# Optimization experiments

Measured on AMD Instinct MI355X. Metric: run time of the kernel, lower is better.

Reference implementation:

```python
import jax, jax.numpy as jnp
import numpy as np

B, S, D = 2, 2048, 1024
H = 16
HD = D // H  # 64
SCALE = HD ** 0.5


def setup_inputs() -> dict:
    key = jax.random.key(0)
    ks = jax.random.split(key, 9)
    std = 1.0 / np.sqrt(D)
    inp = {"x": jax.random.normal(ks[0], (B, S, D), dtype=jnp.float32)}
    names = ["Wq", "Wk", "Wv", "Wo"]
    for i, n in enumerate(names):
        inp[n] = jax.random.uniform(ks[1 + i], (D, D), dtype=jnp.float32, minval=-std, maxval=std)
        inp["b" + n[1]] = jax.random.uniform(ks[5 + i], (D,), dtype=jnp.float32, minval=-std, maxval=std)
    return inp


def reference(x, Wq, Wk, Wv, Wo, bq, bk, bv, bo):
    # QKV projections (torch Linear: y = x @ W.T + b; here W stored as [in, out] already transposed)
    q = x @ Wq + bq
    k = x @ Wk + bk
    v = x @ Wv + bv
    # [B, H, S, HD]
    q = q.reshape(B, S, H, HD).transpose(0, 2, 1, 3)
    k = k.reshape(B, S, H, HD).transpose(0, 2, 1, 3)
    v = v.reshape(B, S, H, HD).transpose(0, 2, 1, 3)
    scores = jnp.einsum("bhqd,bhkd->bhqk", q, k) / SCALE  # [B, H, S, S]
    causal = jnp.tril(jnp.ones((S, S), dtype=bool))
    scores = jnp.where(causal, scores, -jnp.inf)
    attn = jax.nn.softmax(scores, axis=-1)  # dropout p=0.0 (eval)
    ctx = jnp.einsum("bhqk,bhkd->bhqd", attn, v)
    ctx = ctx.transpose(0, 2, 1, 3).reshape(B, S, D)
    return ctx @ Wo + bo
```

## Files before the change

### kernel.cpp

```cpp
#include <hip/hip_runtime.h>


#define S_LEN 2048
#define DMODEL 1024
#define NHEAD 16
#define HDIM 64
#define MROWS 4096

typedef __bf16 bf16x8 __attribute__((ext_vector_type(8)));
typedef float f32x4 __attribute__((ext_vector_type(4)));
typedef float f32x16 __attribute__((ext_vector_type(16)));

__device__ __forceinline__ ushort f2bf(float f) {
  union { float f; unsigned u; } v; v.f = f;
  unsigned r = v.u + 0x7fffu + ((v.u >> 16) & 1u);
  return (ushort)(r >> 16);
}

__device__ __forceinline__ void gload_lds16(const ushort* g, ushort* l) {
  __builtin_amdgcn_global_load_lds(
      (const __attribute__((address_space(1))) void*)g,
      (__attribute__((address_space(3))) void*)l, 16, 0, 0);
}

__device__ __forceinline__ unsigned pack2bf(float lo, float hi) {
  union { __bf16 h[2]; unsigned u; } t;
  t.h[0] = (__bf16)lo; t.h[1] = (__bf16)hi;
  return t.u;
}

#if __has_builtin(__builtin_amdgcn_permlane32_swap)
#define HAVE_PL32 1
__device__ __forceinline__ void pl32sw(unsigned& a, unsigned& b) {
  auto r = __builtin_amdgcn_permlane32_swap((int)a, (int)b, false, false);
  a = (unsigned)r[0];
  b = (unsigned)r[1];
}
#endif

__device__ __forceinline__ float halfcomb_sum(float x) {
#ifdef HAVE_PL32
  unsigned a = __float_as_uint(x), b = a;
  pl32sw(a, b);
  return __uint_as_float(a) + __uint_as_float(b);
#else
  return x + __shfl_xor(x, 32, 64);
#endif
}


__global__ __launch_bounds__(256) void cvt_x(const float* __restrict__ x,
                                             ushort* __restrict__ xb) {
  int i = (blockIdx.x * 256 + threadIdx.x) * 4;
  float4 v = *(const float4*)&x[i];
  ushort4 o;
  o.x = f2bf(v.x); o.y = f2bf(v.y); o.z = f2bf(v.z); o.w = f2bf(v.w);
  *(ushort4*)&xb[i] = o;
}

__global__ __launch_bounds__(256) void cvt_wt(const float* __restrict__ W0,
                                              const float* __restrict__ W1,
                                              const float* __restrict__ W2,
                                              const float* __restrict__ W3,
                                              ushort* __restrict__ out) {
  const float* W = blockIdx.z == 0 ? W0 : blockIdx.z == 1 ? W1
                   : blockIdx.z == 2 ? W2 : W3;
  ushort* WT = out + (size_t)blockIdx.z * DMODEL * DMODEL;
  __shared__ float tile[64][65];
  const int n0 = blockIdx.x * 64, k0 = blockIdx.y * 64;
#pragma unroll
  for (int i = 0; i < 4; ++i) {
    int chunk = i * 256 + threadIdx.x;
    int r = chunk >> 4, c4 = chunk & 15;
    float4 v = *(const float4*)&W[(size_t)(k0 + r) * DMODEL + n0 + c4 * 4];
    tile[r][c4 * 4 + 0] = v.x; tile[r][c4 * 4 + 1] = v.y;
    tile[r][c4 * 4 + 2] = v.z; tile[r][c4 * 4 + 3] = v.w;
  }
  __syncthreads();
#pragma unroll
  for (int i = 0; i < 4; ++i) {
    int chunk = i * 256 + threadIdx.x;
    int r = chunk >> 4, c4 = chunk & 15;
    ushort4 o;
    o.x = f2bf(tile[c4 * 4 + 0][r]); o.y = f2bf(tile[c4 * 4 + 1][r]);
    o.z = f2bf(tile[c4 * 4 + 2][r]); o.w = f2bf(tile[c4 * 4 + 3][r]);
    *(ushort4*)&WT[(size_t)(n0 + r) * DMODEL + k0 + c4 * 4] = o;
  }
}

__global__ __launch_bounds__(256) void trV(const ushort* __restrict__ V,
                                           ushort* __restrict__ Vt) {
  const int bh = blockIdx.z;
  const ushort* src = V + (size_t)bh * S_LEN * HDIM;
  ushort* dst = Vt + (size_t)bh * HDIM * S_LEN;
  __shared__ ushort tile[32][33];
  int s0 = blockIdx.x * 32, h0 = blockIdx.y * 32;
  int tx = threadIdx.x & 31, ty = threadIdx.x >> 5;
#pragma unroll
  for (int i = 0; i < 32; i += 8)
    tile[ty + i][tx] = src[(size_t)(s0 + ty + i) * HDIM + h0 + tx];
  __syncthreads();
#pragma unroll
  for (int i = 0; i < 32; i += 8)
    dst[(size_t)(h0 + ty + i) * S_LEN + s0 + tx] = tile[tx][ty + i];
}

__global__ __launch_bounds__(512) void gemm256(
    const ushort* __restrict__ A, const ushort* __restrict__ Bt,
    const float* __restrict__ b0, const float* __restrict__ b1,
    const float* __restrict__ b2, ushort* __restrict__ outQ,
    ushort* __restrict__ outK, ushort* __restrict__ outV) {
  const int flat = blockIdx.y * 16 + blockIdx.x;
  const int swz = (flat & 7) * 32 + (flat >> 3);
  const int bx = swz & 15, by = swz >> 4;
  const int m0 = bx * 256, n0 = by * 192;

  __shared__ __align__(16) ushort Al[2][256 * 64];
  __shared__ __align__(16) ushort Bl[2][192 * 64];

  const int tid = threadIdx.x;
  const int lane = tid & 63, wid = tid >> 6;
  const int wr = wid >> 2, wc = wid & 3;
  const int fr = lane & 15, hi16 = lane >> 4;

  f32x4 acc[8][3] = {};

#pragma unroll
  for (int l = 0; l < 4; ++l) {
    int chunk = l * 512 + tid;
    int row = chunk >> 3, cpos = chunk & 7;
    int scol = (cpos ^ (row & 7)) * 8;
    gload_lds16(&A[(size_t)(m0 + row) * DMODEL + scol], &Al[0][chunk * 8]);
  }
#pragma unroll
  for (int l = 0; l < 3; ++l) {
    int chunk = l * 512 + tid;
    int row = chunk >> 3, cpos = chunk & 7;
    int scol = (cpos ^ (row & 7)) * 8;
    gload_lds16(&Bt[(size_t)(n0 + row) * DMODEL + scol], &Bl[0][chunk * 8]);
  }
  __syncthreads();

  for (int t = 0; t < 16; ++t) {
    const int bt = t & 1;
    bf16x8 bfr[3];
#pragma unroll
    for (int s = 0; s < 4; ++s) {
      const int kk = s >> 1, mh = s & 1;
      bf16x8 af[4];
#pragma unroll
      for (int q = 0; q < 4; ++q) {
        int rl = wr * 128 + (mh * 4 + q) * 16 + fr;
        af[q] = *(const bf16x8*)&Al[bt][rl * 64 +
                                        ((kk * 4 + hi16) ^ (rl & 7)) * 8];
      }
      if (mh == 0) {
#pragma unroll
        for (int nf = 0; nf < 3; ++nf) {
          int rl = wc * 48 + nf * 16 + fr;
          bfr[nf] = *(const bf16x8*)&Bl[bt][rl * 64 +
                                            ((kk * 4 + hi16) ^ (rl & 7)) * 8];
        }
      }
      if (t + 1 < 16 && s < 2) {
        const int k64 = (t + 1) * 64;
        if (s == 0) {
#pragma unroll
          for (int l = 0; l < 4; ++l) {
            int chunk = l * 512 + tid;
            int row = chunk >> 3, cpos = chunk & 7;
            int scol = (cpos ^ (row & 7)) * 8;
            gload_lds16(&A[(size_t)(m0 + row) * DMODEL + k64 + scol],
                        &Al[bt ^ 1][chunk * 8]);
          }
        } else {
#pragma unroll
          for (int l = 0; l < 3; ++l) {
            int chunk = l * 512 + tid;
            int row = chunk >> 3, cpos = chunk & 7;
            int scol = (cpos ^ (row & 7)) * 8;
            gload_lds16(&Bt[(size_t)(n0 + row) * DMODEL + k64 + scol],
                        &Bl[bt ^ 1][chunk * 8]);
          }
        }
      }
      __builtin_amdgcn_s_barrier();
      __builtin_amdgcn_s_setprio(1);
#pragma unroll
      for (int q = 0; q < 4; ++q)
#pragma unroll
        for (int nf = 0; nf < 3; ++nf)
          acc[mh * 4 + q][nf] = __builtin_amdgcn_mfma_f32_16x16x32_bf16(
              af[q], bfr[nf], acc[mh * 4 + q][nf], 0, 0, 0);
      __builtin_amdgcn_s_setprio(0);
      if (s < 3) __builtin_amdgcn_s_barrier();
    }
    __syncthreads();
  }

#pragma unroll
  for (int mf = 0; mf < 8; ++mf) {
#pragma unroll
    for (int nf = 0; nf < 3; ++nf) {
      int col = n0 + wc * 48 + nf * 16 + fr;
      int z = col >> 10, cw = col & 1023;
      float bval = z == 0 ? b0[cw] : z == 1 ? b1[cw] : b2[cw];
      int h = cw >> 6, hd = cw & (HDIM - 1);
      ushort* dst = (z == 0) ? outQ : (z == 1) ? outK : outV;
#pragma unroll
      for (int rg = 0; rg < 4; ++rg) {
        int row = m0 + wr * 128 + mf * 16 + hi16 * 4 + rg;
        int b = row >> 11, sq = row & (S_LEN - 1);
        float val = acc[mf][nf][rg] + bval;
        dst[(((size_t)(b * NHEAD + h)) * S_LEN + sq) * HDIM + hd] = f2bf(val);
      }
    }
  }
}

__global__ __launch_bounds__(256) void gemm128o(
    const ushort* __restrict__ A, const ushort* __restrict__ Bt,
    const float* __restrict__ b0, float* __restrict__ outB) {
  const int NT = 256;
  const int flat = blockIdx.y * 32 + blockIdx.x;
  const int swz = (flat & 7) * (NT >> 3) + (flat >> 3);
  const int bx = swz & 31, by = swz >> 5;
  const int m0 = bx * 128, n0 = by * 128;

  __shared__ __align__(16) ushort Alds[2][128 * 64];
  __shared__ __align__(16) ushort Blds[2][128 * 64];

  const int tid = threadIdx.x;
  const int lane = tid & 63, w = tid >> 6;
  const int wr = w >> 1, wc = w & 1;
  const int fr = lane & 15, hi16 = lane >> 4;

  f32x4 acc[4][4] = {};

#pragma unroll
  for (int it = 0; it < 4; ++it) {
    int c = it * 256 + tid;
    int row = c >> 3;
    int sc = ((c & 7) ^ (row & 7)) * 8;
    gload_lds16(&A[(size_t)(m0 + row) * DMODEL + sc], &Alds[0][c * 8]);
    gload_lds16(&Bt[(size_t)(n0 + row) * DMODEL + sc], &Blds[0][c * 8]);
  }
  __syncthreads();

  for (int t = 0; t < 16; ++t) {
    const int bt = t & 1;
#pragma unroll
    for (int s = 0; s < 2; ++s) {
      bf16x8 af[4], bfr[4];
#pragma unroll
      for (int i = 0; i < 4; ++i) {
        int row = wr * 64 + i * 16 + fr;
        af[i] = *(const bf16x8*)&Alds[bt][row * 64 +
                                          ((s * 4 + hi16) ^ (row & 7)) * 8];
      }
#pragma unroll
      for (int j = 0; j < 4; ++j) {
        int row = wc * 64 + j * 16 + fr;
        bfr[j] = *(const bf16x8*)&Blds[bt][row * 64 +
                                           ((s * 4 + hi16) ^ (row & 7)) * 8];
      }
      if (t + 1 < 16) {
        const int k64 = (t + 1) * 64;
#pragma unroll
        for (int it = 0; it < 4; ++it) {
          int c = it * 256 + tid;
          int row = c >> 3;
          int sc = ((c & 7) ^ (row & 7)) * 8;
          if (s == 0)
            gload_lds16(&A[(size_t)(m0 + row) * DMODEL + k64 + sc],
                        &Alds[bt ^ 1][c * 8]);
          else
            gload_lds16(&Bt[(size_t)(n0 + row) * DMODEL + k64 + sc],
                        &Blds[bt ^ 1][c * 8]);
        }
      }
      __builtin_amdgcn_s_barrier();
      __builtin_amdgcn_s_setprio(1);
#pragma unroll
      for (int i = 0; i < 4; ++i)
#pragma unroll
        for (int j = 0; j < 4; ++j)
          acc[i][j] = __builtin_amdgcn_mfma_f32_16x16x32_bf16(af[i], bfr[j],
                                                              acc[i][j], 0, 0, 0);
      __builtin_amdgcn_s_setprio(0);
      if (s < 1) __builtin_amdgcn_s_barrier();
    }
    __syncthreads();
  }

#pragma unroll
  for (int i = 0; i < 4; ++i) {
#pragma unroll
    for (int j = 0; j < 4; ++j) {
      int col = n0 + wc * 64 + j * 16 + fr;
      float bval = b0[col];
#pragma unroll
      for (int r = 0; r < 4; ++r) {
        int row = m0 + wr * 64 + i * 16 + hi16 * 4 + r;
        outB[(size_t)row * DMODEL + col] = acc[i][j][r] + bval;
      }
    }
  }
}

__global__ __launch_bounds__(512, 1) void attn8(const ushort* __restrict__ Q,
                                                const ushort* __restrict__ K,
                                                const ushort* __restrict__ Vt,
                                                ushort* __restrict__ ctx) {
  const int blk = blockIdx.x;
  const int w2 = (blk & 7) * 32 + (blk >> 3);
  const int bh = w2 >> 3, ptile = w2 & 7;
  const int b = bh >> 4, h = bh & 15;
  const int tid = threadIdx.x;
  const int lane = tid & 63, wid = tid >> 6;
  const int p = wid >> 2;
  const int wq = wid & 3;
  const int q32 = lane & 31, hi = lane >> 5;
  const bool lo_half = (hi == 0);
  const int tidp = tid & 255;

  const ushort* Qb = Q + (size_t)bh * S_LEN * HDIM;
  const ushort* Kb = K + (size_t)bh * S_LEN * HDIM;
  const ushort* Vb = Vt + (size_t)bh * HDIM * S_LEN;

  __shared__ __align__(16) ushort lds[32768];
  ushort* Klp = lds;
  ushort* Vlp = lds + 16384;
  float* scr = (float*)lds;

  const float C = 0.125f * 1.44269504f;

  for (int ph = 0; ph < 2; ++ph) {
    const int T = ph ? 15 - ptile : ptile;
    const int qbase = T * 128 + wq * 32;
    const int qrow = qbase + q32;
    const int NS = T + 1;

    bf16x8 qf[4];
#pragma unroll
    for (int s = 0; s < 4; ++s)
      qf[s] = *(const bf16x8*)&Qb[(size_t)qrow * HDIM + s * 16 + hi * 8];

    f32x16 oaccA[2] = {}, oaccB[2] = {};
    float lsum = 0.f;

    {
      const int kv = p * 64;
#pragma unroll
      for (int g = 0; g < 2; ++g) {
        int chunk = g * 256 + tidp;
        int row = chunk >> 3, sc = ((chunk & 7) ^ (row & 7)) * 8;
        gload_lds16(&Kb[(size_t)(kv + row) * HDIM + sc],
                    &Klp[(p * 2 + 0) * 4096 + chunk * 8]);
        gload_lds16(&Vb[(size_t)row * S_LEN + kv + sc],
                    &Vlp[(p * 2 + 0) * 4096 + chunk * 8]);
      }
    }
    __syncthreads();

    int buf = 0;
    for (int it = 0; it < NS; ++it) {
      const int s = 2 * it + p;
      const int kv0 = s * 64;

      if (it + 1 < NS) {
        const int kvn = kv0 + 128;
#pragma unroll
        for (int g = 0; g < 2; ++g) {
          int chunk = g * 256 + tidp;
          int row = chunk >> 3, sc = ((chunk & 7) ^ (row & 7)) * 8;
          gload_lds16(&Kb[(size_t)(kvn + row) * HDIM + sc],
                      &Klp[(p * 2 + (buf ^ 1)) * 4096 + chunk * 8]);
          gload_lds16(&Vb[(size_t)row * S_LEN + kvn + sc],
                      &Vlp[(p * 2 + (buf ^ 1)) * 4096 + chunk * 8]);
        }
      }

      if (kv0 <= qbase + 31) {
        const ushort* Kt = &Klp[(p * 2 + buf) * 4096];
        const ushort* Vtl = &Vlp[(p * 2 + buf) * 4096];
        const int rsw = (q32 & 7);

        f32x16 sa[2] = {};
        __builtin_amdgcn_s_setprio(1);
#pragma unroll
        for (int sl = 0; sl < 4; ++sl) {
          bf16x8 kf0 = *(const bf16x8*)&Kt[q32 * 64 + ((sl * 2 + hi) ^ rsw) * 8];
          bf16x8 kf1 = *(const bf16x8*)&Kt[(32 + q32) * 64 +
                                           ((sl * 2 + hi) ^ rsw) * 8];
          sa[0] = __builtin_amdgcn_mfma_f32_32x32x16_bf16(kf0, qf[sl], sa[0],
                                                          0, 0, 0);
          sa[1] = __builtin_amdgcn_mfma_f32_32x32x16_bf16(kf1, qf[sl], sa[1],
                                                          0, 0, 0);
        }
        __builtin_amdgcn_s_setprio(0);

        bf16x8 vf[2][4];
#pragma unroll
        for (int t2 = 0; t2 < 2; ++t2) {
          const int row = t2 * 32 + q32;
#pragma unroll
          for (int sl = 0; sl < 4; ++sl)
            vf[t2][sl] = *(const bf16x8*)&Vtl[row * 64 +
                                              ((sl * 2 + hi) ^ rsw) * 8];
        }

        if (kv0 + 63 > qbase) {
          const int khi = kv0 + 4 * hi;
#pragma unroll
          for (int t = 0; t < 2; ++t)
#pragma unroll
            for (int rr = 0; rr < 16; ++rr) {
              int kg = khi + t * 32 + (rr & 3) + 8 * (rr >> 2);
              if (kg > qrow) sa[t][rr] = -1e30f;
            }
        }

        float psum = 0.f;
#pragma unroll
        for (int t = 0; t < 2; ++t)
#pragma unroll
          for (int rr = 0; rr < 16; ++rr) {
            float pp = __builtin_exp2f(sa[t][rr] * C);
            sa[t][rr] = pp;
            psum += pp;
          }
        lsum += halfcomb_sum(psum);

        __builtin_amdgcn_s_setprio(1);
#pragma unroll
        for (int t = 0; t < 2; ++t) {
#pragma unroll
          for (int half = 0; half < 2; ++half) {
            const int rb = half * 8;
            unsigned a0 = pack2bf(sa[t][rb + 0], sa[t][rb + 1]);
            unsigned a1 = pack2bf(sa[t][rb + 2], sa[t][rb + 3]);
            unsigned b0w = pack2bf(sa[t][rb + 4], sa[t][rb + 5]);
            unsigned b1w = pack2bf(sa[t][rb + 6], sa[t][rb + 7]);
            union { unsigned u[4]; bf16x8 v; } pf;
#ifdef HAVE_PL32
            pl32sw(a0, b0w);
            pl32sw(a1, b1w);
            pf.u[0] = a0; pf.u[1] = a1; pf.u[2] = b0w; pf.u[3] = b1w;
#else
            unsigned xa0 = __shfl_xor(a0, 32, 64);
            unsigned xa1 = __shfl_xor(a1, 32, 64);
            unsigned xb0 = __shfl_xor(b0w, 32, 64);
            unsigned xb1 = __shfl_xor(b1w, 32, 64);
            pf.u[0] = lo_half ? a0 : xb0;
            pf.u[1] = lo_half ? a1 : xb1;
            pf.u[2] = lo_half ? xa0 : b0w;
            pf.u[3] = lo_half ? xa1 : b1w;
#endif
            if (t == 0) {
              oaccA[0] = __builtin_amdgcn_mfma_f32_32x32x16_bf16(
                  vf[0][half], pf.v, oaccA[0], 0, 0, 0);
              oaccA[1] = __builtin_amdgcn_mfma_f32_32x32x16_bf16(
                  vf[1][half], pf.v, oaccA[1], 0, 0, 0);
            } else {
              oaccB[0] = __builtin_amdgcn_mfma_f32_32x32x16_bf16(
                  vf[0][2 + half], pf.v, oaccB[0], 0, 0, 0);
              oaccB[1] = __builtin_amdgcn_mfma_f32_32x32x16_bf16(
                  vf[1][2 + half], pf.v, oaccB[1], 0, 0, 0);
            }
          }
        }
        __builtin_amdgcn_s_setprio(0);
      }

      __syncthreads();
      buf ^= 1;
    }

#pragma unroll
    for (int tt = 0; tt < 2; ++tt)
#pragma unroll
      for (int rr = 0; rr < 16; ++rr) oaccA[tt][rr] += oaccB[tt][rr];

    const int base = (wq * 64 + lane) * 37;
    if (p == 1) {
      scr[base + 0] = lsum;
#pragma unroll
      for (int t = 0; t < 2; ++t)
#pragma unroll
        for (int rr = 0; rr < 16; ++rr)
          scr[base + 1 + t * 16 + rr] = oaccA[t][rr];
    }
    __syncthreads();
    if (p == 0) {
      const float lT = lsum + scr[base + 0];
      const float linv = 1.0f / lT;
      ushort* crow = &ctx[((size_t)(b * S_LEN) + qrow) * DMODEL + h * HDIM];
#pragma unroll
      for (int t = 0; t < 2; ++t)
#pragma unroll
        for (int g2 = 0; g2 < 4; ++g2) {
          ushort4 o;
          float m0 = oaccA[t][g2 * 4 + 0] + scr[base + 1 + t * 16 + g2 * 4 + 0];
          float m1 = oaccA[t][g2 * 4 + 1] + scr[base + 1 + t * 16 + g2 * 4 + 1];
          float m2 = oaccA[t][g2 * 4 + 2] + scr[base + 1 + t * 16 + g2 * 4 + 2];
          float m3 = oaccA[t][g2 * 4 + 3] + scr[base + 1 + t * 16 + g2 * 4 + 3];
          o.x = f2bf(m0 * linv); o.y = f2bf(m1 * linv);
          o.z = f2bf(m2 * linv); o.w = f2bf(m3 * linv);
          *(ushort4*)&crow[t * 32 + g2 * 8 + hi * 4] = o;
        }
    }
    __syncthreads();
  }
}


extern "C" void kernel_launch(void* const* d_in, const int* in_sizes, int n_in,
                              void* d_out, int out_size, void* d_ws,
                              size_t ws_size, hipStream_t stream) {
  const float* x  = (const float*)d_in[0];
  const float* Wq = (const float*)d_in[1];
  const float* bq = (const float*)d_in[2];
  const float* Wk = (const float*)d_in[3];
  const float* bk = (const float*)d_in[4];
  const float* Wv = (const float*)d_in[5];
  const float* bv = (const float*)d_in[6];
  const float* Wo = (const float*)d_in[7];
  const float* bo = (const float*)d_in[8];

  char* ws = (char*)d_ws;
  ushort* Xbf = (ushort*)ws;
  ushort* WT  = (ushort*)(ws + (size_t)8 * 1024 * 1024);
  ushort* QKV = (ushort*)(ws + (size_t)16 * 1024 * 1024);
  ushort* CTX = (ushort*)(ws + (size_t)40 * 1024 * 1024);

  const size_t QKV_ELEMS = (size_t)MROWS * DMODEL;
  const size_t W_ELEMS = (size_t)DMODEL * DMODEL;

  ushort* Qp  = QKV;
  ushort* Kp  = QKV + QKV_ELEMS;
  ushort* Vtp = QKV + 2 * QKV_ELEMS;
  ushort* Vrp = CTX;

  cvt_x<<<4096, 256, 0, stream>>>(x, Xbf);
  cvt_wt<<<dim3(16, 16, 4), 256, 0, stream>>>(Wq, Wk, Wv, Wo, WT);
  gemm256<<<dim3(16, 16), 512, 0, stream>>>(Xbf, WT, bq, bk, bv, Qp, Kp, Vrp);
  trV<<<dim3(64, 2, 32), 256, 0, stream>>>(Vrp, Vtp);
  attn8<<<dim3(256), 512, 0, stream>>>(Qp, Kp, Vtp, CTX);
  gemm128o<<<dim3(32, 8), 256, 0, stream>>>(CTX, WT + 3 * W_ELEMS, bo,
                                            (float*)d_out);
}
```

Measured before the change: 116.0 us.

## Prefetch next K-tile at loop top with vmcnt waits; fold softmax scale into Q

The QKV GEMM now issues all global-to-LDS loads for the next K tile at the start of each iteration and waits on vmcnt for the current tile, replacing the mid-loop staged issue and the per-iteration __syncthreads with s_barrier plus sched_barrier. The softmax scale (1/sqrt(d)·log2e) is folded into the Q projection epilogue, which removes a multiply per score in the attention inner loop. The aim is cleaner load/compute overlap and fewer ALU ops. The risk is that the hand-set vmcnt count must match the number of issued loads, and scaling Q before bf16 rounding changes the numerics slightly.

```diff
diff --git a/kernel.cpp b/kernel.cpp
--- a/kernel.cpp
+++ b/kernel.cpp
@@ -122,27 +122,42 @@
   const int lane = tid & 63, wid = tid >> 6;
   const int wr = wid >> 2, wc = wid & 3;
   const int fr = lane & 15, hi16 = lane >> 4;
+  const float SM_C = 0.125f * 1.44269504f;
 
   f32x4 acc[8][3] = {};
 
-#pragma unroll
-  for (int l = 0; l < 4; ++l) {
-    int chunk = l * 512 + tid;
-    int row = chunk >> 3, cpos = chunk & 7;
-    int scol = (cpos ^ (row & 7)) * 8;
-    gload_lds16(&A[(size_t)(m0 + row) * DMODEL + scol], &Al[0][chunk * 8]);
-  }
-#pragma unroll
-  for (int l = 0; l < 3; ++l) {
-    int chunk = l * 512 + tid;
-    int row = chunk >> 3, cpos = chunk & 7;
-    int scol = (cpos ^ (row & 7)) * 8;
-    gload_lds16(&Bt[(size_t)(n0 + row) * DMODEL + scol], &Bl[0][chunk * 8]);
-  }
-  __syncthreads();
+  auto ISSUE = [&](int k64, int bi) {
+#pragma unroll
+    for (int l = 0; l < 4; ++l) {
+      int chunk = l * 512 + tid;
+      int row = chunk >> 3, cpos = chunk & 7;
+      int scol = (cpos ^ (row & 7)) * 8;
+      gload_lds16(&A[(size_t)(m0 + row) * DMODEL + k64 + scol],
+                  &Al[bi][chunk * 8]);
+    }
+#pragma unroll
+    for (int l = 0; l < 3; ++l) {
+      int chunk = l * 512 + tid;
+      int row = chunk >> 3, cpos = chunk & 7;
+      int scol = (cpos ^ (row & 7)) * 8;
+      gload_lds16(&Bt[(size_t)(n0 + row) * DMODEL + k64 + scol],
+                  &Bl[bi][chunk * 8]);
+    }
+  };
+
+  ISSUE(0, 0);
 
   for (int t = 0; t < 16; ++t) {
     const int bt = t & 1;
+    if (t + 1 < 16) {
+      ISSUE((t + 1) * 64, bt ^ 1);
+      asm volatile("s_waitcnt vmcnt(7)" ::: "memory");
+    } else {
+      asm volatile("s_waitcnt vmcnt(0)" ::: "memory");
+    }
+    __builtin_amdgcn_s_barrier();
+    __builtin_amdgcn_sched_barrier(0);
+
     bf16x8 bfr[3];
 #pragma unroll
     for (int s = 0; s < 4; ++s) {
@@ -162,29 +177,7 @@
                                             ((kk * 4 + hi16) ^ (rl & 7)) * 8];
         }
       }
-      if (t + 1 < 16 && s < 2) {
-        const int k64 = (t + 1) * 64;
-        if (s == 0) {
-#pragma unroll
-          for (int l = 0; l < 4; ++l) {
-            int chunk = l * 512 + tid;
-            int row = chunk >> 3, cpos = chunk & 7;
-            int scol = (cpos ^ (row & 7)) * 8;
-            gload_lds16(&A[(size_t)(m0 + row) * DMODEL + k64 + scol],
-                        &Al[bt ^ 1][chunk * 8]);
-          }
-        } else {
-#pragma unroll
-          for (int l = 0; l < 3; ++l) {
-            int chunk = l * 512 + tid;
-            int row = chunk >> 3, cpos = chunk & 7;
-            int scol = (cpos ^ (row & 7)) * 8;
-            gload_lds16(&Bt[(size_t)(n0 + row) * DMODEL + k64 + scol],
-                        &Bl[bt ^ 1][chunk * 8]);
-          }
-        }
-      }
-      __builtin_amdgcn_s_barrier();
+      if (s > 0) __builtin_amdgcn_s_barrier();
       __builtin_amdgcn_s_setprio(1);
 #pragma unroll
       for (int q = 0; q < 4; ++q)
@@ -193,9 +186,9 @@
           acc[mh * 4 + q][nf] = __builtin_amdgcn_mfma_f32_16x16x32_bf16(
               af[q], bfr[nf], acc[mh * 4 + q][nf], 0, 0, 0);
       __builtin_amdgcn_s_setprio(0);
-      if (s < 3) __builtin_amdgcn_s_barrier();
-    }
-    __syncthreads();
+    }
+    __builtin_amdgcn_s_barrier();
+    __builtin_amdgcn_sched_barrier(0);
   }
 
 #pragma unroll
@@ -207,11 +200,12 @@
       float bval = z == 0 ? b0[cw] : z == 1 ? b1[cw] : b2[cw];
       int h = cw >> 6, hd = cw & (HDIM - 1);
       ushort* dst = (z == 0) ? outQ : (z == 1) ? outK : outV;
+      float sc = (z == 0) ? SM_C : 1.0f;
 #pragma unroll
       for (int rg = 0; rg < 4; ++rg) {
         int row = m0 + wr * 128 + mf * 16 + hi16 * 4 + rg;
         int b = row >> 11, sq = row & (S_LEN - 1);
-        float val = acc[mf][nf][rg] + bval;
+        float val = (acc[mf][nf][rg] + bval) * sc;
         dst[(((size_t)(b * NHEAD + h)) * S_LEN + sq) * HDIM + hd] = f2bf(val);
       }
     }
@@ -333,8 +327,6 @@
   ushort* Vlp = lds + 16384;
   float* scr = (float*)lds;
 
-  const float C = 0.125f * 1.44269504f;
-
   for (int ph = 0; ph < 2; ++ph) {
     const int T = ph ? 15 - ptile : ptile;
     const int qbase = T * 128 + wq * 32;
@@ -426,7 +418,7 @@
         for (int t = 0; t < 2; ++t)
 #pragma unroll
           for (int rr = 0; rr < 16; ++rr) {
-            float pp = __builtin_exp2f(sa[t][rr] * C);
+            float pp = __builtin_exp2f(sa[t][rr]);
             sa[t][rr] = pp;
             psum += pp;
           }
```

Result: no change. 114.1 us (-1.7%).
